# Performance work log

Measured on AMD Instinct MI355X. Metric: run time of the kernel, lower is better.

## Reference

```python
import jax, jax.numpy as jnp
import numpy as np

SCALES = (16, 32, 64, 128)
P = 8
D = 1024
H = 16
DEPTH = 8
MLP = 4096
NCLS = 1000
PB = [(s // P) ** 2 for s in SCALES]            # [4, 16, 64, 256]
BLOCKS = [PB[0] + 1] + PB[1:]                    # [5, 16, 64, 256]
L = sum(BLOCKS)                                  # 341
PATCH_L = sum(PB)                                # 340
PD = P * P * 3                                   # 192
HD = D // H
EPS = 1e-6

# scale id per token (start token belongs to scale 0)
_SID = np.concatenate([np.full(n, k, dtype=np.int32) for k, n in enumerate(BLOCKS)])
# additive block-causal mask: token in scale q may attend to scales <= q
_ALLOW = _SID[None, :] <= _SID[:, None]
MASK = jnp.where(jnp.asarray(_ALLOW), 0.0, -1e30).astype(jnp.float32)  # [L, L]
SID = jnp.asarray(_SID)


def _ln(x):
    m = jnp.mean(x, axis=-1, keepdims=True)
    v = jnp.var(x, axis=-1, keepdims=True)
    return (x - m) / jnp.sqrt(v + EPS)


def _l2n(t):
    n = jnp.sqrt(jnp.sum(t * t, axis=-1, keepdims=True))
    return t / jnp.maximum(n, 1e-12)


def setup_inputs() -> dict:
    key = jax.random.key(0)
    ks = jax.random.split(key, 16)
    s = 0.02
    inp = {
        "patches": jax.random.normal(ks[0], (8, PATCH_L, PD), jnp.float32),
        "labels": jax.random.randint(ks[1], (8,), 0, NCLS),
        "W_patch": s * jax.random.normal(ks[2], (PD, D), jnp.float32),
        "b_patch": jnp.zeros((D,), jnp.float32),
        "pos": s * jax.random.normal(ks[3], (1, L, D), jnp.float32),
        "scale_emb": s * jax.random.normal(ks[4], (len(SCALES), D), jnp.float32),
        "class_emb": s * jax.random.normal(ks[5], (NCLS + 1, D), jnp.float32),
        "ada_W": s * jax.random.normal(ks[6], (DEPTH, D, 6 * D), jnp.float32),
        "ada_b": jnp.zeros((DEPTH, 6 * D), jnp.float32),
        "qkv_W": s * jax.random.normal(ks[7], (DEPTH, D, 3 * D), jnp.float32),
        "qkv_b": jnp.zeros((DEPTH, 3 * D), jnp.float32),
        "q_scale": jnp.zeros((DEPTH, 1, 1, H, 1), jnp.float32),  # log-scale per head
        "proj_W": s * jax.random.normal(ks[8], (DEPTH, D, D), jnp.float32),
        "proj_b": jnp.zeros((DEPTH, D), jnp.float32),
        "fc1_W": s * jax.random.normal(ks[9], (DEPTH, D, MLP), jnp.float32),
        "fc1_b": jnp.zeros((DEPTH, MLP), jnp.float32),
        "fc2_W": s * jax.random.normal(ks[10], (DEPTH, MLP, D), jnp.float32),
        "fc2_b": jnp.zeros((DEPTH, D), jnp.float32),
        "head_ada_W": s * jax.random.normal(ks[11], (D, 2 * D), jnp.float32),
        "head_ada_b": jnp.zeros((2 * D,), jnp.float32),
        "head_W": s * jax.random.normal(ks[12], (D, PD), jnp.float32),
        "head_b": jnp.zeros((PD,), jnp.float32),
    }
    return inp


def reference(patches, labels, W_patch, b_patch, pos, scale_emb, class_emb,
              ada_W, ada_b, qkv_W, qkv_b, q_scale, proj_W, proj_b,
              fc1_W, fc1_b, fc2_W, fc2_b, head_ada_W, head_ada_b, head_W, head_b):
    B = patches.shape[0]
    cond = class_emb[labels]                              # [B, D]
    tok = patches @ W_patch + b_patch                     # [B, PATCH_L, D]
    x = jnp.concatenate([cond[:, None, :], tok], axis=1)  # [B, L, D]
    x = x + pos + scale_emb[SID]

    for i in range(DEPTH):
        ada = jax.nn.silu(cond) @ ada_W[i] + ada_b[i]     # [B, 6D]
        g1, g2, s1, s2, sh1, sh2 = [a[:, None, :] for a in jnp.split(ada, 6, axis=-1)]
        # attention branch
        h = _ln(x) * (s1 + 1.0) + sh1
        qkv = (h @ qkv_W[i] + qkv_b[i]).reshape(B, L, 3, H, HD)
        q, k, v = qkv[:, :, 0], qkv[:, :, 1], qkv[:, :, 2]  # [B, L, H, HD]
        q = _l2n(q) * jnp.exp(q_scale[i])                  # attn_l2_norm
        k = _l2n(k)
        scores = jnp.einsum("bqhd,bkhd->bhqk", q, k) + MASK
        attn = jax.nn.softmax(scores, axis=-1)
        o = jnp.einsum("bhqk,bkhd->bqhd", attn, v).reshape(B, L, D)
        x = x + g1 * (o @ proj_W[i] + proj_b[i])
        # mlp branch
        h2 = _ln(x) * (s2 + 1.0) + sh2
        m = jax.nn.gelu(h2 @ fc1_W[i] + fc1_b[i]) @ fc2_W[i] + fc2_b[i]
        x = x + g2 * m

    ada = jax.nn.silu(cond) @ head_ada_W + head_ada_b     # [B, 2D]
    sc, sh = [a[:, None, :] for a in jnp.split(ada, 2, axis=-1)]
    x = _ln(x) * (sc + 1.0) + sh
    return x @ head_W + head_b                            # [B, L, PD]
```

## Files before the change

### kernel.cpp

```cpp
#include <hip/hip_runtime.h>

typedef unsigned short ushort_t;
typedef __bf16 bf16x8 __attribute__((ext_vector_type(8)));
typedef float f32x4 __attribute__((ext_vector_type(4)));

#define DEV __device__ __forceinline__

DEV ushort_t f2bf(float x) {
  union { float f; unsigned u; } v; v.f = x;
  unsigned r = v.u + 0x7FFFu + ((v.u >> 16) & 1u);
  return (ushort_t)(r >> 16);
}
DEV float bf2f(ushort_t h) {
  union { unsigned u; float f; } v; v.u = (unsigned)h << 16;
  return v.f;
}
DEV int sid_of(int l) { return l < 5 ? 0 : (l < 21 ? 1 : (l < 85 ? 2 : 3)); }
DEV float fast_tanh(float u) { return 1.0f - 2.0f / (__expf(2.0f * u) + 1.0f); }
DEV float gelu_f(float x) {
  float u = 0.7978845608028654f * (x + 0.044715f * x * x * x);
  return 0.5f * x * (1.0f + fast_tanh(u));
}
DEV float silu_f(float x) { return x / (1.0f + __expf(-x)); }
DEV f32x4 mfma16(bf16x8 a, bf16x8 b, f32x4 c) {
  return __builtin_amdgcn_mfma_f32_16x16x32_bf16(a, b, c, 0, 0, 0);
}

DEV void gload16(const void* src, void* dst) {
  __builtin_amdgcn_global_load_lds(
      (const __attribute__((address_space(1))) void*)(uintptr_t)src,
      (__attribute__((address_space(3))) void*)(uintptr_t)dst, 16, 0, 0);
}

__global__ __launch_bounds__(256) void k_cond_x0(
    const int* __restrict__ labels, const float* __restrict__ class_emb,
    const float* __restrict__ pos, const float* __restrict__ semb,
    float* __restrict__ cond, float* __restrict__ x) {
  int b = blockIdx.x, t = threadIdx.x;
  int lab = labels[b];
  float4 cv = *(const float4*)&class_emb[(size_t)lab * 1024 + t * 4];
  *(float4*)&cond[(size_t)b * 1024 + t * 4] = cv;
  float4 pv = *(const float4*)&pos[t * 4];
  float4 sv = *(const float4*)&semb[t * 4];
  float4 xv;
  xv.x = cv.x + pv.x + sv.x; xv.y = cv.y + pv.y + sv.y;
  xv.z = cv.z + pv.z + sv.z; xv.w = cv.w + pv.w + sv.w;
  *(float4*)&x[(size_t)b * 341 * 1024 + t * 4] = xv;
}

__global__ __launch_bounds__(256) void k_convert(const float* __restrict__ src,
                                                 ushort_t* __restrict__ dst, int n4) {
  int i = blockIdx.x * 256 + threadIdx.x;
  if (i < n4) {
    float4 v = *(const float4*)&src[(size_t)i * 4];
    uint2 pk;
    pk.x = (unsigned)f2bf(v.x) | ((unsigned)f2bf(v.y) << 16);
    pk.y = (unsigned)f2bf(v.z) | ((unsigned)f2bf(v.w) << 16);
    *(uint2*)&dst[(size_t)i * 4] = pk;
  }
}

__global__ __launch_bounds__(256) void k_transpose(const float* __restrict__ src,
                                                   ushort_t* __restrict__ dst, int K, int N) {
  __shared__ ushort_t tile[32][33];
  int z = blockIdx.z;
  src += (size_t)z * K * N;
  dst += (size_t)z * K * N;
  int k0 = blockIdx.y * 32, n0 = blockIdx.x * 32;
  int t = threadIdx.x;
  int r = t >> 3, c = (t & 7) * 4;
  float4 v = *(const float4*)&src[(size_t)(k0 + r) * N + n0 + c];
  tile[r][c] = f2bf(v.x); tile[r][c + 1] = f2bf(v.y);
  tile[r][c + 2] = f2bf(v.z); tile[r][c + 3] = f2bf(v.w);
  __syncthreads();
  ushort_t o0 = tile[c][r], o1 = tile[c + 1][r], o2 = tile[c + 2][r], o3 = tile[c + 3][r];
  uint2 pk;
  pk.x = (unsigned)o0 | ((unsigned)o1 << 16);
  pk.y = (unsigned)o2 | ((unsigned)o3 << 16);
  *(uint2*)&dst[(size_t)(n0 + r) * K + k0 + c] = pk;
}

__global__ __launch_bounds__(256) void k_ada(const float* __restrict__ cond,
    const float* __restrict__ ada_W, const float* __restrict__ ada_b,
    const float* __restrict__ hada_W, const float* __restrict__ hada_b,
    float* __restrict__ ada_out, float* __restrict__ hada_out) {
  int gy = blockIdx.y;
  bool head = (gy == 8);
  int Nw = head ? 2048 : 6144;
  int n0 = blockIdx.x * 64;
  if (n0 >= Nw) return;
  __shared__ float sc[8 * 1024];
  __shared__ float red[4][64][8];
  int t = threadIdx.x;
  for (int i = t; i < 2048; i += 256) {
    float4 cv = *(const float4*)&cond[(size_t)i * 4];
    float* d = &sc[i * 4];
    d[0] = silu_f(cv.x); d[1] = silu_f(cv.y); d[2] = silu_f(cv.z); d[3] = silu_f(cv.w);
  }
  __syncthreads();
  const float* W = head ? hada_W : ada_W + (size_t)gy * 1024 * 6144;
  const float* bs = head ? hada_b : ada_b + (size_t)gy * 6144;
  float* op = head ? hada_out : ada_out + (size_t)gy * 8 * 6144;
  int col = n0 + (t & 63), kq = t >> 6;
  float acc[8] = {0.f, 0.f, 0.f, 0.f, 0.f, 0.f, 0.f, 0.f};
  for (int k = kq * 256; k < kq * 256 + 256; ++k) {
    float wv = W[(size_t)k * Nw + col];
#pragma unroll
    for (int b2 = 0; b2 < 8; ++b2) acc[b2] += wv * sc[b2 * 1024 + k];
  }
#pragma unroll
  for (int b2 = 0; b2 < 8; ++b2) red[kq][t & 63][b2] = acc[b2];
  __syncthreads();
  if (t < 64) {
    int colc = n0 + t;
    float bias = bs[colc];
#pragma unroll
    for (int b2 = 0; b2 < 8; ++b2) {
      float v = red[0][t][b2] + red[1][t][b2] + red[2][t][b2] + red[3][t][b2] + bias;
      op[(size_t)b2 * Nw + colc] = v;
    }
  }
}

__global__ __launch_bounds__(256) void k_ln(const float* __restrict__ x,
    ushort_t* __restrict__ hout, const float* __restrict__ ada,
    int stride, int soff, int shoff) {
  int row = blockIdx.x, t = threadIdx.x;
  int b = row / 341;
  const float* xr = x + (size_t)row * 1024;
  float4 xv = *(const float4*)&xr[t * 4];
  float s = xv.x + xv.y + xv.z + xv.w;
  float ss = xv.x * xv.x + xv.y * xv.y + xv.z * xv.z + xv.w * xv.w;
#pragma unroll
  for (int off = 1; off < 64; off <<= 1) { s += __shfl_xor(s, off); ss += __shfl_xor(ss, off); }
  __shared__ float red[8];
  int w = t >> 6, lane = t & 63;
  if (lane == 0) { red[w] = s; red[w + 4] = ss; }
  __syncthreads();
  s = red[0] + red[1] + red[2] + red[3];
  ss = red[4] + red[5] + red[6] + red[7];
  float mean = s * (1.f / 1024.f);
  float var = ss * (1.f / 1024.f) - mean * mean;
  float rstd = rsqrtf(var + 1e-6f);
  const float* ar = ada + (size_t)b * stride;
  float xe[4] = {xv.x, xv.y, xv.z, xv.w};
  ushort_t tmp[4];
#pragma unroll
  for (int j = 0; j < 4; ++j) {
    int n = t * 4 + j;
    float val = (xe[j] - mean) * rstd * (1.f + ar[soff + n]) + ar[shoff + n];
    tmp[j] = f2bf(val);
  }
  uint2 pk;
  pk.x = (unsigned)tmp[0] | ((unsigned)tmp[1] << 16);
  pk.y = (unsigned)tmp[2] | ((unsigned)tmp[3] << 16);
  *(uint2*)&hout[(size_t)row * 1024 + t * 4] = pk;
}

template <int EPI, int BM>
__global__ __launch_bounds__(256, 3) void k_gemm(
    const ushort_t* __restrict__ A, const ushort_t* __restrict__ Bt,
    const float* __restrict__ bias, float* __restrict__ fout,
    ushort_t* __restrict__ bfout, const float* __restrict__ aux,
    float* __restrict__ xres, const float* __restrict__ pos,
    const float* __restrict__ semb, int M, int N, int K) {
  constexpr int NI = (BM == 128) ? 4 : 2;
  constexpr int WNB = (BM == 128) ? 64 : 32;
  __shared__ ushort_t aT[2][BM * 32];
  __shared__ ushort_t bT[2][128 * 32];
  int tid = threadIdx.x;
  int lane = tid & 63, w = tid >> 6;
  int WR = (BM == 128) ? (w >> 1) : 0;
  int WC = (BM == 128) ? (w & 1) : w;

  int gx = gridDim.x;
  int nwg = gx * gridDim.y;
  int orig = blockIdx.y * gx + blockIdx.x;
  int q = nwg >> 3, r8 = nwg & 7;
  int xcd = orig & 7, idx = orig >> 3;
  int lin = (xcd < r8 ? xcd * (q + 1) : r8 * (q + 1) + (xcd - r8) * q) + idx;
  int bx = lin % gx, by = lin / gx;

  int m0 = by * BM, n0 = bx * 128;
  f32x4 acc[4][NI];
#pragma unroll
  for (int i = 0; i < 4; ++i)
#pragma unroll
    for (int j = 0; j < NI; ++j) acc[i][j] = (f32x4){0.f, 0.f, 0.f, 0.f};

  int lrow = lane & 15;
  int csw = (lrow >> 1) & 3;
  int coff = ((lane >> 4) ^ csw) * 8;

  int s_row0 = tid >> 2, s_u = tid & 3;
  int s_c = s_u ^ ((s_row0 >> 1) & 3);
  int aR0 = m0 + s_row0; if (aR0 > M - 1) aR0 = M - 1;
  int bR0 = n0 + s_row0; if (bR0 > N - 1) bR0 = N - 1;
  int aR1 = m0 + s_row0 + 64; if (aR1 > M - 1) aR1 = M - 1;
  int bR1 = n0 + s_row0 + 64; if (bR1 > N - 1) bR1 = N - 1;
  const ushort_t* aSrc0 = A + (size_t)aR0 * K + s_c * 8;
  const ushort_t* aSrc1 = A + (size_t)aR1 * K + s_c * 8;
  const ushort_t* bSrc0 = Bt + (size_t)bR0 * K + s_c * 8;
  const ushort_t* bSrc1 = Bt + (size_t)bR1 * K + s_c * 8;
  int slot0 = w * 512, slot1 = 2048 + w * 512;

  int nsteps = K >> 5;
  auto STAGE = [&](int k0, int buf) {
    gload16(aSrc0 + k0, &aT[buf][slot0]);
    if constexpr (BM == 128) gload16(aSrc1 + k0, &aT[buf][slot1]);
    gload16(bSrc0 + k0, &bT[buf][slot0]);
    gload16(bSrc1 + k0, &bT[buf][slot1]);
  };

  STAGE(0, 0);
  int cur = 0;
  for (int s = 0; s < nsteps; ++s) {
    int kn = (s + 1 < nsteps) ? ((s + 1) << 5) : 0;
    STAGE(kn, cur ^ 1);
    if constexpr (BM == 128)
      asm volatile("s_waitcnt vmcnt(4)" ::: "memory");
    else
      asm volatile("s_waitcnt vmcnt(3)" ::: "memory");
    __builtin_amdgcn_sched_barrier(0);
    __builtin_amdgcn_s_barrier();
    __builtin_amdgcn_sched_barrier(0);
    bf16x8 af[4], bb[NI];
#pragma unroll
    for (int mi = 0; mi < 4; ++mi)
      af[mi] = *(const bf16x8*)&aT[cur][(WR * 64 + mi * 16 + lrow) * 32 + coff];
#pragma unroll
    for (int ni = 0; ni < NI; ++ni)
      bb[ni] = *(const bf16x8*)&bT[cur][(WC * WNB + ni * 16 + lrow) * 32 + coff];
#pragma unroll
    for (int mi = 0; mi < 4; ++mi)
#pragma unroll
      for (int ni = 0; ni < NI; ++ni)
        acc[mi][ni] = mfma16(af[mi], bb[ni], acc[mi][ni]);
    __builtin_amdgcn_sched_barrier(0);
    __builtin_amdgcn_s_barrier();
    __builtin_amdgcn_sched_barrier(0);
    cur ^= 1;
  }

#pragma unroll
  for (int mi = 0; mi < 4; ++mi) {
#pragma unroll
    for (int ni = 0; ni < NI; ++ni) {
#pragma unroll
      for (int r = 0; r < 4; ++r) {
        int gm = m0 + WR * 64 + mi * 16 + (lane >> 4) * 4 + r;
        int gn = n0 + WC * WNB + ni * 16 + lrow;
        if (gm >= M || gn >= N) continue;
        float v = acc[mi][ni][r] + bias[gn];
        if constexpr (EPI == 0) {
          fout[(size_t)gm * N + gn] = v;
        } else if constexpr (EPI == 1) {
          int b = gm / 341;
          size_t xi = (size_t)gm * 1024 + gn;
          xres[xi] += aux[(size_t)b * 6144 + gn] * v;
        } else if constexpr (EPI == 2) {
          bfout[(size_t)gm * N + gn] = f2bf(gelu_f(v));
        } else if constexpr (EPI == 4) {
          int b = gm / 340, l = gm % 340 + 1;
          float val = v + pos[(size_t)l * 1024 + gn] + semb[(size_t)sid_of(l) * 1024 + gn];
          xres[((size_t)(b * 341 + l)) * 1024 + gn] = val;
        } else if constexpr (EPI == 5) {
          bfout[(size_t)gm * N + gn] = f2bf(v);
        }
      }
    }
  }
}

__global__ __launch_bounds__(256) void k_qknorm(
    const ushort_t* __restrict__ qkv, const float* __restrict__ qscale,
    ushort_t* __restrict__ qa, ushort_t* __restrict__ ka, ushort_t* __restrict__ vt) {
  int c = blockIdx.x, h = blockIdx.y, b = blockIdx.z;
  int t = threadIdx.x, lane = t & 63, w = t >> 6;
  float qse = __expf(qscale[h]);
  size_t bh = (size_t)(b * 16 + h);
#pragma unroll 4
  for (int it = 0; it < 16; ++it) {
    int l = c * 64 + w * 16 + it;
    bool valid = l < 341;
    float q = 0.f, k = 0.f;
    if (valid) {
      size_t rb = ((size_t)(b * 341 + l)) * 3072 + h * 64 + lane;
      q = bf2f(qkv[rb]);
      k = bf2f(qkv[rb + 1024]);
    }
    float q2 = q * q, k2 = k * k;
#pragma unroll
    for (int off = 1; off < 64; off <<= 1) { q2 += __shfl_xor(q2, off); k2 += __shfl_xor(k2, off); }
    float qn = valid ? q / fmaxf(sqrtf(q2), 1e-12f) * qse : 0.f;
    float kn = valid ? k / fmaxf(sqrtf(k2), 1e-12f) : 0.f;
    size_t ob = (bh * 384 + l) * 64 + lane;
    qa[ob] = f2bf(qn);
    ka[ob] = f2bf(kn);
  }
  __shared__ ushort_t vt_s[64 * 72];
#pragma unroll
  for (int i = 0; i < 2; ++i) {
    int vid = t + 256 * i;
    int rl = vid >> 3, dc = (vid & 7) * 8;
    int l = c * 64 + rl;
    uint4 vv = {0u, 0u, 0u, 0u};
    if (l < 341) vv = *(const uint4*)&qkv[((size_t)(b * 341 + l)) * 3072 + 2048 + h * 64 + dc];
    *(uint4*)&vt_s[rl * 72 + dc] = vv;
  }
  __syncthreads();
  {
    int d = t >> 2, lseg = (t & 3) * 16;
    ushort_t tmp[16];
#pragma unroll
    for (int j = 0; j < 16; ++j) tmp[j] = vt_s[(lseg + j) * 72 + d];
    ushort_t* dp = vt + (bh * 64 + d) * 384 + c * 64 + lseg;
    uint4 s0, s1;
    s0.x = (unsigned)tmp[0] | ((unsigned)tmp[1] << 16);
    s0.y = (unsigned)tmp[2] | ((unsigned)tmp[3] << 16);
    s0.z = (unsigned)tmp[4] | ((unsigned)tmp[5] << 16);
    s0.w = (unsigned)tmp[6] | ((unsigned)tmp[7] << 16);
    s1.x = (unsigned)tmp[8] | ((unsigned)tmp[9] << 16);
    s1.y = (unsigned)tmp[10] | ((unsigned)tmp[11] << 16);
    s1.z = (unsigned)tmp[12] | ((unsigned)tmp[13] << 16);
    s1.w = (unsigned)tmp[14] | ((unsigned)tmp[15] << 16);
    *(uint4*)dp = s0;
    *(uint4*)(dp + 8) = s1;
  }
}

__global__ __launch_bounds__(256) void k_attn(
    const ushort_t* __restrict__ qa, const ushort_t* __restrict__ ka,
    const ushort_t* __restrict__ vt, ushort_t* __restrict__ o) {
  int qt = blockIdx.x, h = blockIdx.y, b = blockIdx.z;
  int t = threadIdx.x, lane = t & 63, w = t >> 6;
  int q0 = qt * 64;
  size_t bh = (size_t)(b * 16 + h);
  __shared__ ushort_t qT[64 * 72], kT[64 * 72], vT[64 * 72];
  __shared__ ushort_t pT[4][16 * 72];
#pragma unroll
  for (int i = 0; i < 2; ++i) {
    int vid = t + 256 * i;
    int row = vid >> 3, seg = (vid & 7) * 8;
    uint4 v = *(const uint4*)&qa[(bh * 384 + q0 + row) * 64 + seg];
    *(uint4*)&qT[row * 72 + seg] = v;
  }
  int lrow = lane & 15, lk8 = (lane >> 4) * 8;
  int sq[4];
  float mrun[4], lsum[4];
  f32x4 accO[4];
#pragma unroll
  for (int r = 0; r < 4; ++r) {
    int lq = q0 + w * 16 + (lane >> 4) * 4 + r;
    sq[r] = sid_of(lq < 341 ? lq : 340);
    mrun[r] = -1e30f;
    lsum[r] = 0.f;
  }
#pragma unroll
  for (int d = 0; d < 4; ++d) accO[d] = (f32x4){0.f, 0.f, 0.f, 0.f};
  int sq_max = sid_of(q0 + 63 < 341 ? q0 + 63 : 340);
  for (int c = 0; c < 6; ++c) {
    if (sid_of(c * 64) > sq_max) continue;
    __syncthreads();
#pragma unroll
    for (int i = 0; i < 2; ++i) {
      int vid = t + 256 * i;
      int row = vid >> 3, seg = (vid & 7) * 8;
      uint4 kv = *(const uint4*)&ka[(bh * 384 + c * 64 + row) * 64 + seg];
      *(uint4*)&kT[row * 72 + seg] = kv;
      uint4 vv = *(const uint4*)&vt[(bh * 64 + row) * 384 + c * 64 + seg];
      *(uint4*)&vT[row * 72 + seg] = vv;
    }
    __syncthreads();
    f32x4 sf[4];
#pragma unroll
    for (int nf = 0; nf < 4; ++nf) sf[nf] = (f32x4){0.f, 0.f, 0.f, 0.f};
#pragma unroll
    for (int ks = 0; ks < 2; ++ks) {
      bf16x8 aq = *(const bf16x8*)&qT[(w * 16 + lrow) * 72 + ks * 32 + lk8];
#pragma unroll
      for (int nf = 0; nf < 4; ++nf) {
        bf16x8 bk = *(const bf16x8*)&kT[(nf * 16 + lrow) * 72 + ks * 32 + lk8];
        sf[nf] = mfma16(aq, bk, sf[nf]);
      }
    }
#pragma unroll
    for (int nf = 0; nf < 4; ++nf) {
      int lk = c * 64 + nf * 16 + lrow;
      int sk = lk < 341 ? sid_of(lk) : 9;
#pragma unroll
      for (int r = 0; r < 4; ++r)
        if (sk > sq[r]) sf[nf][r] = -1e30f;
    }
    float rs[4];
#pragma unroll
    for (int r = 0; r < 4; ++r) {
      float m = sf[0][r];
      m = fmaxf(m, sf[1][r]); m = fmaxf(m, sf[2][r]); m = fmaxf(m, sf[3][r]);
#pragma unroll
      for (int off = 1; off < 16; off <<= 1) m = fmaxf(m, __shfl_xor(m, off));
      float mn = fmaxf(mrun[r], m);
      float scl = __expf(mrun[r] - mn);
      mrun[r] = mn;
      lsum[r] *= scl;
#pragma unroll
      for (int d = 0; d < 4; ++d) accO[d][r] *= scl;
      rs[r] = 0.f;
    }
    ushort_t* pw = &pT[w][0];
#pragma unroll
    for (int nf = 0; nf < 4; ++nf) {
#pragma unroll
      for (int r = 0; r < 4; ++r) {
        float p = __expf(sf[nf][r] - mrun[r]);
        rs[r] += p;
        pw[((lane >> 4) * 4 + r) * 72 + nf * 16 + lrow] = f2bf(p);
      }
    }
#pragma unroll
    for (int r = 0; r < 4; ++r) {
      float sum = rs[r];
#pragma unroll
      for (int off = 1; off < 16; off <<= 1) sum += __shfl_xor(sum, off);
      lsum[r] += sum;
    }
#pragma unroll
    for (int ks = 0; ks < 2; ++ks) {
      bf16x8 ap = *(const bf16x8*)&pw[lrow * 72 + ks * 32 + lk8];
#pragma unroll
      for (int d = 0; d < 4; ++d) {
        bf16x8 bv = *(const bf16x8*)&vT[(d * 16 + lrow) * 72 + ks * 32 + lk8];
        accO[d] = mfma16(ap, bv, accO[d]);
      }
    }
  }
#pragma unroll
  for (int d = 0; d < 4; ++d) {
#pragma unroll
    for (int r = 0; r < 4; ++r) {
      int lq = q0 + w * 16 + (lane >> 4) * 4 + r;
      if (lq < 341) {
        float ov = accO[d][r] / fmaxf(lsum[r], 1e-30f);
        o[((size_t)(b * 341 + lq)) * 1024 + h * 64 + d * 16 + lrow] = f2bf(ov);
      }
    }
  }
}

extern "C" void kernel_launch(void* const* d_in, const int* in_sizes, int n_in,
                              void* d_out, int out_size, void* d_ws, size_t ws_size,
                              hipStream_t stream) {
  const float* patches   = (const float*)d_in[0];
  const int*   labels    = (const int*)d_in[1];
  const float* W_patch   = (const float*)d_in[2];
  const float* b_patch   = (const float*)d_in[3];
  const float* pos       = (const float*)d_in[4];
  const float* scale_emb = (const float*)d_in[5];
  const float* class_emb = (const float*)d_in[6];
  const float* ada_W     = (const float*)d_in[7];
  const float* ada_b     = (const float*)d_in[8];
  const float* qkv_W     = (const float*)d_in[9];
  const float* qkv_b     = (const float*)d_in[10];
  const float* q_scale   = (const float*)d_in[11];
  const float* proj_W    = (const float*)d_in[12];
  const float* proj_b    = (const float*)d_in[13];
  const float* fc1_W     = (const float*)d_in[14];
  const float* fc1_b     = (const float*)d_in[15];
  const float* fc2_W     = (const float*)d_in[16];
  const float* fc2_b     = (const float*)d_in[17];
  const float* hada_W    = (const float*)d_in[18];
  const float* hada_b    = (const float*)d_in[19];
  const float* head_W    = (const float*)d_in[20];
  const float* head_b    = (const float*)d_in[21];
  (void)in_sizes; (void)n_in; (void)out_size; (void)ws_size;

  char* wsb = (char*)d_ws;
  size_t off = 0;
  auto alloc = [&](size_t bytes) -> void* {
    void* p = wsb + off;
    off = (off + bytes + 255) & ~(size_t)255;
    return p;
  };

  float*    f_cond   = (float*)alloc(8 * 1024 * 4);
  float*    f_ada    = (float*)alloc((size_t)8 * 8 * 6144 * 4);
  float*    f_hada   = (float*)alloc(8 * 2048 * 4);
  float*    f_x      = (float*)alloc((size_t)2728 * 1024 * 4);
  ushort_t* u_h      = (ushort_t*)alloc((size_t)2728 * 1024 * 2);
  ushort_t* u_qkv    = (ushort_t*)alloc((size_t)2728 * 3072 * 2);
  ushort_t* u_qa     = (ushort_t*)alloc((size_t)128 * 384 * 64 * 2);
  ushort_t* u_ka     = (ushort_t*)alloc((size_t)128 * 384 * 64 * 2);
  ushort_t* u_vt     = (ushort_t*)alloc((size_t)128 * 64 * 384 * 2);
  ushort_t* u_o      = (ushort_t*)alloc((size_t)2728 * 1024 * 2);
  ushort_t* u_mid    = (ushort_t*)alloc((size_t)2728 * 4096 * 2);
  ushort_t* u_patch  = (ushort_t*)alloc((size_t)2720 * 192 * 2);
  ushort_t* u_qkvt   = (ushort_t*)alloc((size_t)8 * 3072 * 1024 * 2);
  ushort_t* u_projt  = (ushort_t*)alloc((size_t)8 * 1024 * 1024 * 2);
  ushort_t* u_fc1t   = (ushort_t*)alloc((size_t)8 * 4096 * 1024 * 2);
  ushort_t* u_fc2t   = (ushort_t*)alloc((size_t)8 * 1024 * 4096 * 2);
  ushort_t* u_wpt    = (ushort_t*)alloc((size_t)1024 * 192 * 2);
  ushort_t* u_wht    = (ushort_t*)alloc((size_t)192 * 1024 * 2);

  const int MT = 22;
  const int MT64 = 43;

  k_cond_x0<<<8, 256, 0, stream>>>(labels, class_emb, pos, scale_emb, f_cond, f_x);
  k_transpose<<<dim3(32, 6, 1), 256, 0, stream>>>(W_patch, u_wpt, 192, 1024);
  k_transpose<<<dim3(6, 32, 1), 256, 0, stream>>>(head_W, u_wht, 1024, 192);
  k_convert<<<510, 256, 0, stream>>>(patches, u_patch, 130560);
  k_ada<<<dim3(96, 9), 256, 0, stream>>>(f_cond, ada_W, ada_b, hada_W, hada_b, f_ada, f_hada);
  k_transpose<<<dim3(96, 32, 8), 256, 0, stream>>>(qkv_W, u_qkvt, 1024, 3072);
  k_transpose<<<dim3(32, 32, 8), 256, 0, stream>>>(proj_W, u_projt, 1024, 1024);
  k_transpose<<<dim3(128, 32, 8), 256, 0, stream>>>(fc1_W, u_fc1t, 1024, 4096);
  k_transpose<<<dim3(32, 128, 8), 256, 0, stream>>>(fc2_W, u_fc2t, 4096, 1024);

  k_gemm<4, 128><<<dim3(8, MT), 256, 0, stream>>>(u_patch, u_wpt, b_patch, nullptr, nullptr,
                                                  nullptr, f_x, pos, scale_emb, 2720, 1024, 192);

  for (int i = 0; i < 8; ++i) {
    const float* adaL = f_ada + (size_t)i * 8 * 6144;
    k_ln<<<2728, 256, 0, stream>>>(f_x, u_h, adaL, 6144, 2048, 4096);
    k_gemm<5, 128><<<dim3(24, MT), 256, 0, stream>>>(u_h, u_qkvt + (size_t)i * 3072 * 1024,
                                                     qkv_b + (size_t)i * 3072, nullptr, u_qkv,
                                                     nullptr, nullptr, nullptr, nullptr,
                                                     2728, 3072, 1024);
    k_qknorm<<<dim3(6, 16, 8), 256, 0, stream>>>(u_qkv, q_scale + (size_t)i * 16, u_qa, u_ka, u_vt);
    k_attn<<<dim3(6, 16, 8), 256, 0, stream>>>(u_qa, u_ka, u_vt, u_o);
    k_gemm<1, 64><<<dim3(8, MT64), 256, 0, stream>>>(u_o, u_projt + (size_t)i * 1024 * 1024,
                                                     proj_b + (size_t)i * 1024, nullptr,
                                                     nullptr, adaL, f_x, nullptr, nullptr,
                                                     2728, 1024, 1024);
    k_ln<<<2728, 256, 0, stream>>>(f_x, u_h, adaL, 6144, 3072, 5120);
    k_gemm<2, 128><<<dim3(32, MT), 256, 0, stream>>>(u_h, u_fc1t + (size_t)i * 4096 * 1024,
                                                     fc1_b + (size_t)i * 4096, nullptr,
                                                     u_mid, nullptr, nullptr, nullptr, nullptr,
                                                     2728, 4096, 1024);
    k_gemm<1, 64><<<dim3(8, MT64), 256, 0, stream>>>(u_mid, u_fc2t + (size_t)i * 4096 * 1024,
                                                     fc2_b + (size_t)i * 1024, nullptr,
                                                     nullptr, adaL + 1024, f_x, nullptr, nullptr,
                                                     2728, 1024, 4096);
  }

  k_ln<<<2728, 256, 0, stream>>>(f_x, u_h, f_hada, 2048, 0, 1024);
  k_gemm<0, 64><<<dim3(2, MT64), 256, 0, stream>>>(u_h, u_wht, head_b, (float*)d_out, nullptr,
                                                   nullptr, nullptr, nullptr, nullptr,
                                                   2728, 192, 1024);
}
```

Baseline: 2.033 ms.

## Fuse QK l2-norm into QKV GEMM epilogue, split-K fc2/head GEMMs, transpose V in attention

Drops the separate qknorm kernel. The QKV GEMM epilogue now applies bias and per-head L2 normalization with the q scale, using a 16-lane shuffle reduction. The attention kernel reads q/k/v directly from the packed qkv buffer and transposes V through shared memory, with setprio around the MFMA blocks. The fc2 and head GEMMs become split-K with fp32 partials, reduced by a new combine kernel that applies bias, gating and the residual. This removes a kernel launch and intermediate traffic and raises parallelism for the small-N GEMMs, at the cost of extra partial-buffer traffic and an added sync in attention.

```diff
diff --git a/kernel.cpp b/kernel.cpp
--- a/kernel.cpp
+++ b/kernel.cpp
@@ -163,7 +163,7 @@
     const float* __restrict__ bias, float* __restrict__ fout,
     ushort_t* __restrict__ bfout, const float* __restrict__ aux,
     float* __restrict__ xres, const float* __restrict__ pos,
-    const float* __restrict__ semb, int M, int N, int K) {
+    const float* __restrict__ semb, int M, int N, int K, int KS) {
   constexpr int NI = (BM == 128) ? 4 : 2;
   constexpr int WNB = (BM == 128) ? 64 : 32;
   __shared__ ushort_t aT[2][BM * 32];
@@ -182,6 +182,7 @@
   int bx = lin % gx, by = lin / gx;
 
   int m0 = by * BM, n0 = bx * 128;
+  int kbase = blockIdx.z * KS;
   f32x4 acc[4][NI];
 #pragma unroll
   for (int i = 0; i < 4; ++i)
@@ -198,13 +199,13 @@
   int bR0 = n0 + s_row0; if (bR0 > N - 1) bR0 = N - 1;
   int aR1 = m0 + s_row0 + 64; if (aR1 > M - 1) aR1 = M - 1;
   int bR1 = n0 + s_row0 + 64; if (bR1 > N - 1) bR1 = N - 1;
-  const ushort_t* aSrc0 = A + (size_t)aR0 * K + s_c * 8;
-  const ushort_t* aSrc1 = A + (size_t)aR1 * K + s_c * 8;
-  const ushort_t* bSrc0 = Bt + (size_t)bR0 * K + s_c * 8;
-  const ushort_t* bSrc1 = Bt + (size_t)bR1 * K + s_c * 8;
+  const ushort_t* aSrc0 = A + (size_t)aR0 * K + kbase + s_c * 8;
+  const ushort_t* aSrc1 = A + (size_t)aR1 * K + kbase + s_c * 8;
+  const ushort_t* bSrc0 = Bt + (size_t)bR0 * K + kbase + s_c * 8;
+  const ushort_t* bSrc1 = Bt + (size_t)bR1 * K + kbase + s_c * 8;
   int slot0 = w * 512, slot1 = 2048 + w * 512;
 
-  int nsteps = K >> 5;
+  int nsteps = KS >> 5;
   auto STAGE = [&](int k0, int buf) {
     gload16(aSrc0 + k0, &aT[buf][slot0]);
     if constexpr (BM == 128) gload16(aSrc1 + k0, &aT[buf][slot1]);
@@ -242,107 +243,117 @@
     cur ^= 1;
   }
 
-#pragma unroll
-  for (int mi = 0; mi < 4; ++mi) {
-#pragma unroll
-    for (int ni = 0; ni < NI; ++ni) {
+  if constexpr (EPI == 6) {
+    int nb = n0 + WC * 64;
+    int gh = nb >> 6;
+    float qse = (gh < 16) ? __expf(aux[gh]) : 1.0f;
+    bool dn = gh < 32;
+#pragma unroll
+    for (int mi = 0; mi < 4; ++mi) {
 #pragma unroll
       for (int r = 0; r < 4; ++r) {
+        float vv[4]; float ss = 0.f;
+#pragma unroll
+        for (int ni = 0; ni < 4; ++ni) {
+          vv[ni] = acc[mi][ni][r] + bias[nb + ni * 16 + lrow];
+          ss += vv[ni] * vv[ni];
+        }
+        if (dn) {
+          ss += __shfl_xor(ss, 1); ss += __shfl_xor(ss, 2);
+          ss += __shfl_xor(ss, 4); ss += __shfl_xor(ss, 8);
+          float rn = qse / fmaxf(sqrtf(ss), 1e-12f);
+#pragma unroll
+          for (int ni = 0; ni < 4; ++ni) vv[ni] *= rn;
+        }
         int gm = m0 + WR * 64 + mi * 16 + (lane >> 4) * 4 + r;
-        int gn = n0 + WC * WNB + ni * 16 + lrow;
-        if (gm >= M || gn >= N) continue;
-        float v = acc[mi][ni][r] + bias[gn];
-        if constexpr (EPI == 0) {
-          fout[(size_t)gm * N + gn] = v;
-        } else if constexpr (EPI == 1) {
-          int b = gm / 341;
-          size_t xi = (size_t)gm * 1024 + gn;
-          xres[xi] += aux[(size_t)b * 6144 + gn] * v;
-        } else if constexpr (EPI == 2) {
-          bfout[(size_t)gm * N + gn] = f2bf(gelu_f(v));
-        } else if constexpr (EPI == 4) {
-          int b = gm / 340, l = gm % 340 + 1;
-          float val = v + pos[(size_t)l * 1024 + gn] + semb[(size_t)sid_of(l) * 1024 + gn];
-          xres[((size_t)(b * 341 + l)) * 1024 + gn] = val;
-        } else if constexpr (EPI == 5) {
-          bfout[(size_t)gm * N + gn] = f2bf(v);
+        if (gm < M) {
+#pragma unroll
+          for (int ni = 0; ni < 4; ++ni)
+            bfout[(size_t)gm * N + nb + ni * 16 + lrow] = f2bf(vv[ni]);
         }
       }
     }
-  }
-}
-
-__global__ __launch_bounds__(256) void k_qknorm(
-    const ushort_t* __restrict__ qkv, const float* __restrict__ qscale,
-    ushort_t* __restrict__ qa, ushort_t* __restrict__ ka, ushort_t* __restrict__ vt) {
-  int c = blockIdx.x, h = blockIdx.y, b = blockIdx.z;
-  int t = threadIdx.x, lane = t & 63, w = t >> 6;
-  float qse = __expf(qscale[h]);
-  size_t bh = (size_t)(b * 16 + h);
-#pragma unroll 4
-  for (int it = 0; it < 16; ++it) {
-    int l = c * 64 + w * 16 + it;
-    bool valid = l < 341;
-    float q = 0.f, k = 0.f;
-    if (valid) {
-      size_t rb = ((size_t)(b * 341 + l)) * 3072 + h * 64 + lane;
-      q = bf2f(qkv[rb]);
-      k = bf2f(qkv[rb + 1024]);
-    }
-    float q2 = q * q, k2 = k * k;
-#pragma unroll
-    for (int off = 1; off < 64; off <<= 1) { q2 += __shfl_xor(q2, off); k2 += __shfl_xor(k2, off); }
-    float qn = valid ? q / fmaxf(sqrtf(q2), 1e-12f) * qse : 0.f;
-    float kn = valid ? k / fmaxf(sqrtf(k2), 1e-12f) : 0.f;
-    size_t ob = (bh * 384 + l) * 64 + lane;
-    qa[ob] = f2bf(qn);
-    ka[ob] = f2bf(kn);
-  }
-  __shared__ ushort_t vt_s[64 * 72];
-#pragma unroll
-  for (int i = 0; i < 2; ++i) {
-    int vid = t + 256 * i;
-    int rl = vid >> 3, dc = (vid & 7) * 8;
-    int l = c * 64 + rl;
-    uint4 vv = {0u, 0u, 0u, 0u};
-    if (l < 341) vv = *(const uint4*)&qkv[((size_t)(b * 341 + l)) * 3072 + 2048 + h * 64 + dc];
-    *(uint4*)&vt_s[rl * 72 + dc] = vv;
-  }
-  __syncthreads();
-  {
-    int d = t >> 2, lseg = (t & 3) * 16;
-    ushort_t tmp[16];
-#pragma unroll
-    for (int j = 0; j < 16; ++j) tmp[j] = vt_s[(lseg + j) * 72 + d];
-    ushort_t* dp = vt + (bh * 64 + d) * 384 + c * 64 + lseg;
-    uint4 s0, s1;
-    s0.x = (unsigned)tmp[0] | ((unsigned)tmp[1] << 16);
-    s0.y = (unsigned)tmp[2] | ((unsigned)tmp[3] << 16);
-    s0.z = (unsigned)tmp[4] | ((unsigned)tmp[5] << 16);
-    s0.w = (unsigned)tmp[6] | ((unsigned)tmp[7] << 16);
-    s1.x = (unsigned)tmp[8] | ((unsigned)tmp[9] << 16);
-    s1.y = (unsigned)tmp[10] | ((unsigned)tmp[11] << 16);
-    s1.z = (unsigned)tmp[12] | ((unsigned)tmp[13] << 16);
-    s1.w = (unsigned)tmp[14] | ((unsigned)tmp[15] << 16);
-    *(uint4*)dp = s0;
-    *(uint4*)(dp + 8) = s1;
+  } else {
+#pragma unroll
+    for (int mi = 0; mi < 4; ++mi) {
+#pragma unroll
+      for (int ni = 0; ni < NI; ++ni) {
+#pragma unroll
+        for (int r = 0; r < 4; ++r) {
+          int gm = m0 + WR * 64 + mi * 16 + (lane >> 4) * 4 + r;
+          int gn = n0 + WC * WNB + ni * 16 + lrow;
+          if (gm >= M || gn >= N) continue;
+          if constexpr (EPI == 7) {
+            fout[(size_t)blockIdx.z * M * N + (size_t)gm * N + gn] = acc[mi][ni][r];
+          } else {
+            float v = acc[mi][ni][r] + bias[gn];
+            if constexpr (EPI == 1) {
+              int b = gm / 341;
+              xres[(size_t)gm * 1024 + gn] += aux[(size_t)b * 6144 + gn] * v;
+            } else if constexpr (EPI == 2) {
+              bfout[(size_t)gm * N + gn] = f2bf(gelu_f(v));
+            } else if constexpr (EPI == 4) {
+              int b = gm / 340, l = gm % 340 + 1;
+              float val = v + pos[(size_t)l * 1024 + gn] + semb[(size_t)sid_of(l) * 1024 + gn];
+              xres[((size_t)(b * 341 + l)) * 1024 + gn] = val;
+            }
+          }
+        }
+      }
+    }
+  }
+}
+
+template <int MODE>
+__global__ __launch_bounds__(256) void k_comb(const float* __restrict__ p,
+    const float* __restrict__ bias, const float* __restrict__ aux,
+    float* __restrict__ xres, float* __restrict__ out, int N, int nsplit) {
+  int row = blockIdx.x, t = threadIdx.x;
+  size_t stride = (size_t)2728 * N;
+  if constexpr (MODE == 0) {
+    int c = t * 4;
+    float4 s = *(const float4*)&p[(size_t)row * N + c];
+    for (int sp = 1; sp < nsplit; ++sp) {
+      float4 qq = *(const float4*)&p[sp * stride + (size_t)row * N + c];
+      s.x += qq.x; s.y += qq.y; s.z += qq.z; s.w += qq.w;
+    }
+    float4 bv = *(const float4*)&bias[c];
+    int b = row / 341;
+    const float* ar = aux + (size_t)b * 6144 + c;
+    float4 xv = *(float4*)&xres[(size_t)row * 1024 + c];
+    xv.x += ar[0] * (s.x + bv.x);
+    xv.y += ar[1] * (s.y + bv.y);
+    xv.z += ar[2] * (s.z + bv.z);
+    xv.w += ar[3] * (s.w + bv.w);
+    *(float4*)&xres[(size_t)row * 1024 + c] = xv;
+  } else {
+    if (t < 48) {
+      int c = t * 4;
+      float4 s = *(const float4*)&p[(size_t)row * N + c];
+      for (int sp = 1; sp < nsplit; ++sp) {
+        float4 qq = *(const float4*)&p[sp * stride + (size_t)row * N + c];
+        s.x += qq.x; s.y += qq.y; s.z += qq.z; s.w += qq.w;
+      }
+      float4 bv = *(const float4*)&bias[c];
+      s.x += bv.x; s.y += bv.y; s.z += bv.z; s.w += bv.w;
+      *(float4*)&out[(size_t)row * N + c] = s;
+    }
   }
 }
 
 __global__ __launch_bounds__(256) void k_attn(
-    const ushort_t* __restrict__ qa, const ushort_t* __restrict__ ka,
-    const ushort_t* __restrict__ vt, ushort_t* __restrict__ o) {
+    const ushort_t* __restrict__ qkv, ushort_t* __restrict__ o) {
   int qt = blockIdx.x, h = blockIdx.y, b = blockIdx.z;
   int t = threadIdx.x, lane = t & 63, w = t >> 6;
   int q0 = qt * 64;
-  size_t bh = (size_t)(b * 16 + h);
-  __shared__ ushort_t qT[64 * 72], kT[64 * 72], vT[64 * 72];
+  __shared__ ushort_t qT[64 * 72], kT[64 * 72], vS[64 * 72], vT[64 * 72];
   __shared__ ushort_t pT[4][16 * 72];
 #pragma unroll
   for (int i = 0; i < 2; ++i) {
     int vid = t + 256 * i;
     int row = vid >> 3, seg = (vid & 7) * 8;
-    uint4 v = *(const uint4*)&qa[(bh * 384 + q0 + row) * 64 + seg];
+    int l = q0 + row; if (l > 340) l = 340;
+    uint4 v = *(const uint4*)&qkv[((size_t)(b * 341 + l)) * 3072 + h * 64 + seg];
     *(uint4*)&qT[row * 72 + seg] = v;
   }
   int lrow = lane & 15, lk8 = (lane >> 4) * 8;
@@ -359,22 +370,28 @@
 #pragma unroll
   for (int d = 0; d < 4; ++d) accO[d] = (f32x4){0.f, 0.f, 0.f, 0.f};
   int sq_max = sid_of(q0 + 63 < 341 ? q0 + 63 : 340);
+  int vd = t >> 2, vlseg = (t & 3) * 16;
   for (int c = 0; c < 6; ++c) {
     if (sid_of(c * 64) > sq_max) continue;
-    __syncthreads();
 #pragma unroll
     for (int i = 0; i < 2; ++i) {
       int vid = t + 256 * i;
       int row = vid >> 3, seg = (vid & 7) * 8;
-      uint4 kv = *(const uint4*)&ka[(bh * 384 + c * 64 + row) * 64 + seg];
+      int l = c * 64 + row; if (l > 340) l = 340;
+      size_t base = ((size_t)(b * 341 + l)) * 3072 + h * 64 + seg;
+      uint4 kv = *(const uint4*)&qkv[base + 1024];
+      uint4 vv = *(const uint4*)&qkv[base + 2048];
       *(uint4*)&kT[row * 72 + seg] = kv;
-      uint4 vv = *(const uint4*)&vt[(bh * 64 + row) * 384 + c * 64 + seg];
-      *(uint4*)&vT[row * 72 + seg] = vv;
+      *(uint4*)&vS[row * 72 + seg] = vv;
     }
     __syncthreads();
+    ushort_t tmp[16];
+#pragma unroll
+    for (int j = 0; j < 16; ++j) tmp[j] = vS[(vlseg + j) * 72 + vd];
     f32x4 sf[4];
 #pragma unroll
     for (int nf = 0; nf < 4; ++nf) sf[nf] = (f32x4){0.f, 0.f, 0.f, 0.f};
+    __builtin_amdgcn_s_setprio(1);
 #pragma unroll
     for (int ks = 0; ks < 2; ++ks) {
       bf16x8 aq = *(const bf16x8*)&qT[(w * 16 + lrow) * 72 + ks * 32 + lk8];
@@ -384,6 +401,7 @@
         sf[nf] = mfma16(aq, bk, sf[nf]);
       }
     }
+    __builtin_amdgcn_s_setprio(0);
 #pragma unroll
     for (int nf = 0; nf < 4; ++nf) {
       int lk = c * 64 + nf * 16 + lrow;
@@ -424,6 +442,21 @@
       for (int off = 1; off < 16; off <<= 1) sum += __shfl_xor(sum, off);
       lsum[r] += sum;
     }
+    {
+      uint4 s0, s1;
+      s0.x = (unsigned)tmp[0] | ((unsigned)tmp[1] << 16);
+      s0.y = (unsigned)tmp[2] | ((unsigned)tmp[3] << 16);
+      s0.z = (unsigned)tmp[4] | ((unsigned)tmp[5] << 16);
+      s0.w = (unsigned)tmp[6] | ((unsigned)tmp[7] << 16);
+      s1.x = (unsigned)tmp[8] | ((unsigned)tmp[9] << 16);
+      s1.y = (unsigned)tmp[10] | ((unsigned)tmp[11] << 16);
+      s1.z = (unsigned)tmp[12] | ((unsigned)tmp[13] << 16);
+      s1.w = (unsigned)tmp[14] | ((unsigned)tmp[15] << 16);
+      *(uint4*)&vT[vd * 72 + vlseg] = s0;
+      *(uint4*)&vT[vd * 72 + vlseg + 8] = s1;
+    }
+    __syncthreads();
+    __builtin_amdgcn_s_setprio(1);
 #pragma unroll
     for (int ks = 0; ks < 2; ++ks) {
       bf16x8 ap = *(const bf16x8*)&pw[lrow * 72 + ks * 32 + lk8];
@@ -433,6 +466,7 @@
         accO[d] = mfma16(ap, bv, accO[d]);
       }
     }
+    __builtin_amdgcn_s_setprio(0);
   }
 #pragma unroll
   for (int d = 0; d < 4; ++d) {
@@ -488,11 +522,9 @@
   float*    f_x      = (float*)alloc((size_t)2728 * 1024 * 4);
   ushort_t* u_h      = (ushort_t*)alloc((size_t)2728 * 1024 * 2);
   ushort_t* u_qkv    = (ushort_t*)alloc((size_t)2728 * 3072 * 2);
-  ushort_t* u_qa     = (ushort_t*)alloc((size_t)128 * 384 * 64 * 2);
-  ushort_t* u_ka     = (ushort_t*)alloc((size_t)128 * 384 * 64 * 2);
-  ushort_t* u_vt     = (ushort_t*)alloc((size_t)128 * 64 * 384 * 2);
   ushort_t* u_o      = (ushort_t*)alloc((size_t)2728 * 1024 * 2);
   ushort_t* u_mid    = (ushort_t*)alloc((size_t)2728 * 4096 * 2);
+  float*    f_part   = (float*)alloc((size_t)2 * 2728 * 1024 * 4);
   ushort_t* u_patch  = (ushort_t*)alloc((size_t)2720 * 192 * 2);
   ushort_t* u_qkvt   = (ushort_t*)alloc((size_t)8 * 3072 * 1024 * 2);
   ushort_t* u_projt  = (ushort_t*)alloc((size_t)8 * 1024 * 1024 * 2);
@@ -515,34 +547,36 @@
   k_transpose<<<dim3(32, 128, 8), 256, 0, stream>>>(fc2_W, u_fc2t, 4096, 1024);
 
   k_gemm<4, 128><<<dim3(8, MT), 256, 0, stream>>>(u_patch, u_wpt, b_patch, nullptr, nullptr,
-                                                  nullptr, f_x, pos, scale_emb, 2720, 1024, 192);
+                                                  nullptr, f_x, pos, scale_emb, 2720, 1024, 192, 192);
 
   for (int i = 0; i < 8; ++i) {
     const float* adaL = f_ada + (size_t)i * 8 * 6144;
     k_ln<<<2728, 256, 0, stream>>>(f_x, u_h, adaL, 6144, 2048, 4096);
-    k_gemm<5, 128><<<dim3(24, MT), 256, 0, stream>>>(u_h, u_qkvt + (size_t)i * 3072 * 1024,
+    k_gemm<6, 128><<<dim3(24, MT), 256, 0, stream>>>(u_h, u_qkvt + (size_t)i * 3072 * 1024,
                                                      qkv_b + (size_t)i * 3072, nullptr, u_qkv,
-                                                     nullptr, nullptr, nullptr, nullptr,
-                                                     2728, 3072, 1024);
-    k_qknorm<<<dim3(6, 16, 8), 256, 0, stream>>>(u_qkv, q_scale + (size_t)i * 16, u_qa, u_ka, u_vt);
-    k_attn<<<dim3(6, 16, 8), 256, 0, stream>>>(u_qa, u_ka, u_vt, u_o);
+                                                     q_scale + (size_t)i * 16, nullptr, nullptr,
+                                                     nullptr, 2728, 3072, 1024, 1024);
+    k_attn<<<dim3(6, 16, 8), 256, 0, stream>>>(u_qkv, u_o);
     k_gemm<1, 64><<<dim3(8, MT64), 256, 0, stream>>>(u_o, u_projt + (size_t)i * 1024 * 1024,
                                                      proj_b + (size_t)i * 1024, nullptr,
                                                      nullptr, adaL, f_x, nullptr, nullptr,
-                                                     2728, 1024, 1024);
+                                                     2728, 1024, 1024, 1024);
     k_ln<<<2728, 256, 0, stream>>>(f_x, u_h, adaL, 6144, 3072, 5120);
     k_gemm<2, 128><<<dim3(32, MT), 256, 0, stream>>>(u_h, u_fc1t + (size_t)i * 4096 * 1024,
                                                      fc1_b + (size_t)i * 4096, nullptr,
                                                      u_mid, nullptr, nullptr, nullptr, nullptr,
-                                                     2728, 4096, 1024);
-    k_gemm<1, 64><<<dim3(8, MT64), 256, 0, stream>>>(u_mid, u_fc2t + (size_t)i * 4096 * 1024,
-                                                     fc2_b + (size_t)i * 1024, nullptr,
-                                                     nullptr, adaL + 1024, f_x, nullptr, nullptr,
-                                                     2728, 1024, 4096);
+                                                     2728, 4096, 1024, 1024);
+    k_gemm<7, 64><<<dim3(8, MT64, 2), 256, 0, stream>>>(u_mid, u_fc2t + (size_t)i * 4096 * 1024,
+                                                        nullptr, f_part,
+                                                        nullptr, nullptr, nullptr, nullptr, nullptr,
+                                                        2728, 1024, 4096, 2048);
+    k_comb<0><<<2728, 256, 0, stream>>>(f_part, fc2_b + (size_t)i * 1024, adaL + 1024,
+                                        f_x, nullptr, 1024, 2);
   }
 
   k_ln<<<2728, 256, 0, stream>>>(f_x, u_h, f_hada, 2048, 0, 1024);
-  k_gemm<0, 64><<<dim3(2, MT64), 256, 0, stream>>>(u_h, u_wht, head_b, (float*)d_out, nullptr,
-                                                   nullptr, nullptr, nullptr, nullptr,
-                                                   2728, 192, 1024);
-}
+  k_gemm<7, 64><<<dim3(2, MT64, 4), 256, 0, stream>>>(u_h, u_wht, nullptr, f_part, nullptr,
+                                                      nullptr, nullptr, nullptr, nullptr,
+                                                      2728, 192, 1024, 256);
+  k_comb<1><<<2728, 256, 0, stream>>>(f_part, head_b, nullptr, nullptr, (float*)d_out, 192, 4);
+}
```

Result: faster. 1.809 ms (-11.0%).
